# Kernel optimization log

Hardware: AMD Instinct MI355X
Metric: run time of the kernel (lower is better)

Reference implementation:

```python
import jax, jax.numpy as jnp
import numpy as np

LATENT_CH = 64  # feature_ch // 8


def conv1x1(x, w):
    # Conv2dLayer with kernel_size=1, bias=False, activation='linear':
    # weight_gain = 1/sqrt(in_channels * 1)
    gain = 1.0 / np.sqrt(w.shape[1])
    return jnp.einsum('bchw,oc->bohw', x, w * gain)


def casual_attention(q, k, v):
    # q,k,v: [B, C, N] / [B, C, M]; score = q^T k, softmax over keys, out = score @ v^T
    score = jnp.einsum('bcn,bcm->bnm', q, k)
    score = jax.nn.softmax(score, axis=-1)
    return jnp.einsum('bnm,bcm->bnc', score, v)  # [B, N, C]


def reference(feature_map, concepts, w_theta, w_phi, w_g, w_o, gamma_sa, gamma_moca):
    B, C, H, W = feature_map.shape
    L = LATENT_CH
    HW = H * W

    # ---- SelfAttention ----
    th = conv1x1(feature_map, w_theta).reshape(B, L, HW)
    ph = conv1x1(feature_map, w_phi).reshape(B, L, HW)
    g = conv1x1(feature_map, w_g).reshape(B, L, HW)
    # torch does .view(-1, L, H, W) on a [B, HW, L] tensor -> raw memory reinterpret
    lat = casual_attention(th, ph, g).reshape(B, L, H, W)
    sa_out = gamma_sa * conv1x1(lat, w_o) + feature_map

    # ---- MomentumConceptAttention (theta and o shared with SA, trainable_conv=False) ----
    enc = conv1x1(sa_out, w_theta).reshape(B, L, HW)
    phi_c = concepts.T[None]                      # [1, L, P]  (torch.no_grad on concepts)
    phi_c = jnp.broadcast_to(phi_c, (B, L, concepts.shape[0]))
    lat2 = casual_attention(enc, phi_c, phi_c).reshape(B, L, H, W)
    out = gamma_moca * conv1x1(lat2, w_o) + sa_out
    return out


def setup_inputs() -> dict:
    key = jax.random.key(0)
    ks = jax.random.split(key, 8)
    B, C, H, W = 8, 512, 64, 64
    L, P = LATENT_CH, 256
    return {
        'feature_map': jax.random.normal(ks[0], (B, C, H, W), jnp.float32),
        'concepts': jax.random.normal(ks[1], (P, L), jnp.float32),
        'w_theta': jax.random.normal(ks[2], (L, C), jnp.float32),
        'w_phi': jax.random.normal(ks[3], (L, C), jnp.float32),
        'w_g': jax.random.normal(ks[4], (L, C), jnp.float32),
        'w_o': jax.random.normal(ks[5], (C, L), jnp.float32),
        'gamma_sa': jnp.float32(0.1),
        'gamma_moca': jnp.float32(0.1),
    }
```

## Files before the change

### kernel.cpp

```cpp
#include <hip/hip_runtime.h>
#include <math.h>

#define HW   4096
#define CINP 512
#define LCH  64

typedef short bf8 __attribute__((ext_vector_type(8)));
typedef float f4  __attribute__((ext_vector_type(4)));

__device__ __forceinline__ unsigned short f2bf(float x) {
    union { float f; unsigned int u; } v; v.f = x;
    return (unsigned short)((v.u + 0x7fffu + ((v.u >> 16) & 1u)) >> 16);
}
__device__ __forceinline__ bf8 ldbf8(const unsigned short* p) {
    uint4 u = *(const uint4*)p;
    return __builtin_bit_cast(bf8, u);
}

__global__ __launch_bounds__(256) void precast(
    const float* __restrict__ wt, const float* __restrict__ wp,
    const float* __restrict__ wg, const float* __restrict__ wo,
    const float* __restrict__ conc,
    unsigned short* __restrict__ WB, unsigned short* __restrict__ WO,
    unsigned short* __restrict__ CK, unsigned short* __restrict__ CV)
{
    const float gain = 0.04419417382415922f;
    int id = blockIdx.x * 256 + threadIdx.x;
    if (id < 98304) {
        int o = id >> 9, k = id & 511;
        const float* w = (o < 64) ? wt : (o < 128) ? wp : wg;
        WB[id] = f2bf(w[(o & 63) * 512 + k] * gain);
    } else if (id < 131072) {
        int j = id - 98304;
        WO[j] = f2bf(wo[j]);
    } else if (id < 147456) {
        int j = id - 131072;
        CK[j] = f2bf(conc[j]);
    } else if (id < 163840) {
        int j = id - 147456;
        int l = j >> 8, m = j & 255;
        CV[j] = f2bf(conc[m * 64 + l]);
    }
}

__global__ __launch_bounds__(256) void cast_transpose(const float* __restrict__ x,
                                                      unsigned short* __restrict__ XT)
{
    __shared__ unsigned short Lb[64][72];
    const int t  = threadIdx.x;
    const int n0 = blockIdx.x * 64, c0 = blockIdx.y * 64, b = blockIdx.z;
    const float* xb = x + ((size_t)b * CINP + c0) * HW + n0;
    const int cc = t >> 4, n4 = (t & 15) * 4;
    #pragma unroll
    for (int i = 0; i < 4; i++) {
        int c = cc + i * 16;
        float4 v = *(const float4*)(xb + (size_t)c * HW + n4);
        Lb[n4 + 0][c] = f2bf(v.x);
        Lb[n4 + 1][c] = f2bf(v.y);
        Lb[n4 + 2][c] = f2bf(v.z);
        Lb[n4 + 3][c] = f2bf(v.w);
    }
    __syncthreads();
    const int n = t & 63, cb0 = t >> 6;
    unsigned short* orow = XT + ((size_t)b * HW + n0 + n) * CINP + c0;
    #pragma unroll
    for (int i = 0; i < 2; i++) {
        int cb = cb0 + i * 4;
        *(uint4*)(orow + cb * 8) = *(const uint4*)&Lb[n][cb * 8];
    }
}

__global__ __launch_bounds__(256) void lat_transpose(const unsigned short* __restrict__ A,
                                                     unsigned short* __restrict__ LT)
{
    __shared__ unsigned short Ls[64][72];
    const int t = threadIdx.x, s0 = blockIdx.x * 64, b = blockIdx.y;
    const unsigned short* ab = A + (size_t)b * LCH * HW;
    #pragma unroll
    for (int it = 0; it < 2; it++) {
        int c = (t >> 3) + it * 32, s8 = (t & 7) * 8;
        union { uint4 u; unsigned short s[8]; } v;
        v.u = *(const uint4*)(ab + (size_t)c * HW + s0 + s8);
        #pragma unroll
        for (int i = 0; i < 8; i++) Ls[s8 + i][c] = v.s[i];
    }
    __syncthreads();
    unsigned short* ob = LT + ((size_t)b * HW + s0) * LCH;
    #pragma unroll
    for (int it = 0; it < 2; it++) {
        int s = (t >> 3) + it * 32, c8 = (t & 7);
        *(uint4*)(ob + (size_t)s * LCH + c8 * 8) = *(const uint4*)&Ls[s][c8 * 8];
    }
}

template <int NRT>
__global__ __launch_bounds__(256) void qkv_gemm(unsigned short* XT,
                                                const unsigned short* __restrict__ WB,
                                                unsigned short* __restrict__ VL)
{
    const int t = threadIdx.x;
    const int wave = t >> 6, lane = t & 63, quad = lane >> 4, lidx = lane & 15;
    const int b = blockIdx.y;
    const int ncol = blockIdx.x * 64 + wave * 16 + lidx;
    unsigned short* xrow = XT + ((size_t)b * HW + ncol) * CINP;

    f4 acc[NRT];
    #pragma unroll
    for (int r = 0; r < NRT; r++) acc[r] = (f4){0.f, 0.f, 0.f, 0.f};

    for (int kk = 0; kk < 16; kk++) {
        const int k0 = kk * 32 + quad * 8;
        bf8 bq = ldbf8(xrow + k0);
        #pragma unroll
        for (int rt = 0; rt < NRT; rt++) {
            bf8 aw = ldbf8(WB + (size_t)(rt * 16 + lidx) * CINP + k0);
            acc[rt] = __builtin_amdgcn_mfma_f32_16x16x32_bf16(aw, bq, acc[rt], 0, 0, 0);
        }
    }

    #pragma unroll
    for (int rt = 0; rt < NRT; rt++) {
        if (rt < 8) {
            union { unsigned short s[4]; uint2 u; } pk;
            #pragma unroll
            for (int r = 0; r < 4; r++) pk.s[r] = f2bf(acc[rt][r]);
            int off = (rt < 4) ? (rt * 16 + quad * 4) : (64 + (rt - 4) * 16 + quad * 4);
            *(uint2*)(xrow + off) = pk.u;
        } else {
            #pragma unroll
            for (int r = 0; r < 4; r++) {
                int l = (rt - 8) * 16 + quad * 4 + r;
                VL[((size_t)b * LCH + l) * HW + ncol] = f2bf(acc[rt][r]);
            }
        }
    }
}

__global__ __launch_bounds__(64) void flash(
    const unsigned short* Qb, size_t qbat,
    const unsigned short* Kb, size_t krow, size_t kbat,
    const unsigned short* Vb, size_t vrow, size_t vbat,
    unsigned short* __restrict__ Aout, int nkeys)
{
    __shared__ __align__(16) unsigned short Ps[2][32][40];

    const int lane = threadIdx.x, quad = lane >> 4, lidx = lane & 15;
    const int b = blockIdx.y, q0 = blockIdx.x * 32;
    const unsigned short* qp = Qb + (size_t)b * qbat;
    const unsigned short* kp = Kb + (size_t)b * kbat;
    const unsigned short* vp = Vb + (size_t)b * vbat;

    bf8 qa[2][2];
    #pragma unroll
    for (int qb = 0; qb < 2; qb++)
        #pragma unroll
        for (int kh = 0; kh < 2; kh++)
            qa[qb][kh] = ldbf8(qp + (size_t)(q0 + qb * 16 + lidx) * CINP + kh * 32 + quad * 8);

    f4 O[2][4];
    float Lp[2][4];
    #pragma unroll
    for (int qb = 0; qb < 2; qb++) {
        #pragma unroll
        for (int lt = 0; lt < 4; lt++) O[qb][lt] = (f4){0.f, 0.f, 0.f, 0.f};
        #pragma unroll
        for (int r = 0; r < 4; r++) Lp[qb][r] = 0.f;
    }

    const int ntiles = nkeys >> 5;
    #pragma unroll 2
    for (int tl = 0; tl < ntiles; tl++) {
        const int m0 = tl * 32;
        const unsigned short* kr0 = kp + (size_t)(m0 + lidx) * krow + quad * 8;
        const unsigned short* kr1 = kp + (size_t)(m0 + 16 + lidx) * krow + quad * 8;
        bf8 kf00 = ldbf8(kr0), kf01 = ldbf8(kr0 + 32);
        bf8 kf10 = ldbf8(kr1), kf11 = ldbf8(kr1 + 32);

        f4 S[2][2];
        #pragma unroll
        for (int qb = 0; qb < 2; qb++) {
            S[qb][0] = (f4){0.f, 0.f, 0.f, 0.f};
            S[qb][1] = (f4){0.f, 0.f, 0.f, 0.f};
            S[qb][0] = __builtin_amdgcn_mfma_f32_16x16x32_bf16(qa[qb][0], kf00, S[qb][0], 0, 0, 0);
            S[qb][0] = __builtin_amdgcn_mfma_f32_16x16x32_bf16(qa[qb][1], kf01, S[qb][0], 0, 0, 0);
            S[qb][1] = __builtin_amdgcn_mfma_f32_16x16x32_bf16(qa[qb][0], kf10, S[qb][1], 0, 0, 0);
            S[qb][1] = __builtin_amdgcn_mfma_f32_16x16x32_bf16(qa[qb][1], kf11, S[qb][1], 0, 0, 0);
        }

        const int pb = tl & 1;
        #pragma unroll
        for (int qb = 0; qb < 2; qb++)
            #pragma unroll
            for (int ms = 0; ms < 2; ms++)
                #pragma unroll
                for (int r = 0; r < 4; r++) {
                    float p = __expf(S[qb][ms][r]);
                    Lp[qb][r] += p;
                    Ps[pb][qb * 16 + quad * 4 + r][ms * 16 + lidx] = f2bf(p);
                }

        bf8 pf0 = *(const bf8*)&Ps[pb][lidx][quad * 8];
        bf8 pf1 = *(const bf8*)&Ps[pb][16 + lidx][quad * 8];

        #pragma unroll
        for (int lt = 0; lt < 4; lt++) {
            bf8 vf = ldbf8(vp + (size_t)(lt * 16 + lidx) * vrow + m0 + quad * 8);
            O[0][lt] = __builtin_amdgcn_mfma_f32_16x16x32_bf16(pf0, vf, O[0][lt], 0, 0, 0);
            O[1][lt] = __builtin_amdgcn_mfma_f32_16x16x32_bf16(pf1, vf, O[1][lt], 0, 0, 0);
        }
    }

    #pragma unroll
    for (int qb = 0; qb < 2; qb++) {
        float inv[4];
        #pragma unroll
        for (int r = 0; r < 4; r++) {
            float s = Lp[qb][r];
            s += __shfl_xor(s, 1);
            s += __shfl_xor(s, 2);
            s += __shfl_xor(s, 4);
            s += __shfl_xor(s, 8);
            inv[r] = 1.f / s;
        }
        #pragma unroll
        for (int lt = 0; lt < 4; lt++)
            #pragma unroll
            for (int r = 0; r < 4; r++) {
                size_t n = (size_t)b * HW + q0 + qb * 16 + quad * 4 + r;
                Aout[n * LCH + lt * 16 + lidx] = f2bf(O[qb][lt][r] * inv[r]);
            }
    }
}

__global__ __launch_bounds__(256) void conv_o(const unsigned short* __restrict__ LT,
                                              const unsigned short* __restrict__ WO,
                                              const float* __restrict__ res,
                                              const float* __restrict__ gamma_p,
                                              float* __restrict__ out,
                                              unsigned short* ST)
{
    const int t = threadIdx.x;
    const int wave = t >> 6, lane = t & 63, quad = lane >> 4, lidx = lane & 15;
    const int b = blockIdx.z, o0 = blockIdx.y * 64;
    const int scol = blockIdx.x * 64 + wave * 16 + lidx;
    const unsigned short* arow = LT + ((size_t)b * HW + scol) * LCH;

    f4 acc[4];
    #pragma unroll
    for (int ot = 0; ot < 4; ot++) acc[ot] = (f4){0.f, 0.f, 0.f, 0.f};

    #pragma unroll
    for (int kh = 0; kh < 2; kh++) {
        bf8 bq = ldbf8(arow + kh * 32 + quad * 8);
        #pragma unroll
        for (int ot = 0; ot < 4; ot++) {
            bf8 af = ldbf8(WO + (size_t)(o0 + ot * 16 + lidx) * LCH + kh * 32 + quad * 8);
            acc[ot] = __builtin_amdgcn_mfma_f32_16x16x32_bf16(af, bq, acc[ot], 0, 0, 0);
        }
    }

    const float scale = gamma_p[0] * 0.125f;
    #pragma unroll
    for (int ot = 0; ot < 4; ot++) {
        float v[4];
        #pragma unroll
        for (int r = 0; r < 4; r++) {
            size_t idx = ((size_t)b * CINP + o0 + ot * 16 + quad * 4 + r) * HW + scol;
            v[r] = fmaf(scale, acc[ot][r], res[idx]);
            out[idx] = v[r];
        }
        if (ST) {
            union { unsigned short s[4]; uint2 u; } pk;
            #pragma unroll
            for (int r = 0; r < 4; r++) pk.s[r] = f2bf(v[r]);
            *(uint2*)(ST + ((size_t)b * HW + scol) * CINP + o0 + ot * 16 + quad * 4) = pk.u;
        }
    }
}

extern "C" void kernel_launch(void* const* d_in, const int* in_sizes, int n_in,
                              void* d_out, int out_size, void* d_ws, size_t ws_size,
                              hipStream_t stream)
{
    const float* f    = (const float*)d_in[0];
    const float* conc = (const float*)d_in[1];
    const float* wt   = (const float*)d_in[2];
    const float* wp   = (const float*)d_in[3];
    const float* wg   = (const float*)d_in[4];
    const float* wo   = (const float*)d_in[5];
    const float* gsa  = (const float*)d_in[6];
    const float* gmo  = (const float*)d_in[7];
    float* out = (float*)d_out;

    char* ws = (char*)d_ws;
    unsigned short* XT = (unsigned short*)ws;
    unsigned short* VL = (unsigned short*)(ws + ((size_t)32 << 20));
    unsigned short* LT = VL;
    unsigned short* A1 = (unsigned short*)(ws + ((size_t)36 << 20));
    unsigned short* WB = (unsigned short*)(ws + ((size_t)40 << 20));
    unsigned short* WO = WB + 192 * 512;
    unsigned short* CK = WO + 512 * 64;
    unsigned short* CV = CK + 256 * 64;

    dim3 blk256(256), blk64(64);

    precast<<<640, blk256, 0, stream>>>(wt, wp, wg, wo, conc, WB, WO, CK, CV);
    cast_transpose<<<dim3(64, 8, 8), blk256, 0, stream>>>(f, XT);

    qkv_gemm<12><<<dim3(64, 8), blk256, 0, stream>>>(XT, WB, VL);
    flash<<<dim3(128, 8), blk64, 0, stream>>>(
        XT, (size_t)HW * CINP,
        XT + 64, CINP, (size_t)HW * CINP,
        VL, HW, (size_t)LCH * HW,
        A1, HW);
    lat_transpose<<<dim3(64, 8), blk256, 0, stream>>>(A1, LT);
    conv_o<<<dim3(64, 8, 8), blk256, 0, stream>>>(LT, WO, f, gsa, out, XT );

    qkv_gemm<4><<<dim3(64, 8), blk256, 0, stream>>>(XT , WB , nullptr);
    flash<<<dim3(128, 8), blk64, 0, stream>>>(
        XT, (size_t)HW * CINP,
        CK, LCH, 0,
        CV, 256, 0,
        A1 , 256);
    lat_transpose<<<dim3(64, 8), blk256, 0, stream>>>(A1, LT);
    conv_o<<<dim3(64, 8, 8), blk256, 0, stream>>>(LT, WO, out, gmo, out, nullptr);
}
```

Measured before the change: 416.8 us.

## Split flash attention keys across four waves with LDS reduction

The flash kernel now runs 256 threads per block, and each of four waves processes a quarter of the key tiles for the same 32 queries. Partial output accumulators and row sums are written to shared memory and summed by wave 0 before normalization. This raises the number of active waves to better fill the GPU and hide memory latency. In exchange it adds LDS traffic, two block barriers and extra registers, and it only works when the key count divides into 128-key chunks.

```diff
diff --git a/kernel.cpp b/kernel.cpp
--- a/kernel.cpp
+++ b/kernel.cpp
@@ -136,16 +136,21 @@
     }
 }
 
-__global__ __launch_bounds__(64) void flash(
+__global__ __launch_bounds__(256) void flash(
     const unsigned short* Qb, size_t qbat,
     const unsigned short* Kb, size_t krow, size_t kbat,
     const unsigned short* Vb, size_t vrow, size_t vbat,
     unsigned short* __restrict__ Aout, int nkeys)
 {
-    __shared__ __align__(16) unsigned short Ps[2][32][40];
-
-    const int lane = threadIdx.x, quad = lane >> 4, lidx = lane & 15;
+    __shared__ __align__(16) char smem[31488];
+
+    const int t = threadIdx.x;
+    const int wave = t >> 6, lane = t & 63, quad = lane >> 4, lidx = lane & 15;
     const int b = blockIdx.y, q0 = blockIdx.x * 32;
+
+    unsigned short (*Ps)[32][40] = (unsigned short (*)[32][40])(smem + wave * 5120);
+    float (*Red)[64][41] = (float (*)[64][41])smem;
+
     const unsigned short* qp = Qb + (size_t)b * qbat;
     const unsigned short* kp = Kb + (size_t)b * kbat;
     const unsigned short* vp = Vb + (size_t)b * vbat;
@@ -167,10 +172,11 @@
         for (int r = 0; r < 4; r++) Lp[qb][r] = 0.f;
     }
 
-    const int ntiles = nkeys >> 5;
+    const int tpw = nkeys >> 7;
+    const int tbase = wave * tpw;
     #pragma unroll 2
-    for (int tl = 0; tl < ntiles; tl++) {
-        const int m0 = tl * 32;
+    for (int tt = 0; tt < tpw; tt++) {
+        const int m0 = (tbase + tt) * 32;
         const unsigned short* kr0 = kp + (size_t)(m0 + lidx) * krow + quad * 8;
         const unsigned short* kr1 = kp + (size_t)(m0 + 16 + lidx) * krow + quad * 8;
         bf8 kf00 = ldbf8(kr0), kf01 = ldbf8(kr0 + 32);
@@ -187,7 +193,7 @@
             S[qb][1] = __builtin_amdgcn_mfma_f32_16x16x32_bf16(qa[qb][1], kf11, S[qb][1], 0, 0, 0);
         }
 
-        const int pb = tl & 1;
+        const int pb = tt & 1;
         #pragma unroll
         for (int qb = 0; qb < 2; qb++)
             #pragma unroll
@@ -210,25 +216,59 @@
         }
     }
 
-    #pragma unroll
-    for (int qb = 0; qb < 2; qb++) {
-        float inv[4];
-        #pragma unroll
-        for (int r = 0; r < 4; r++) {
-            float s = Lp[qb][r];
-            s += __shfl_xor(s, 1);
-            s += __shfl_xor(s, 2);
-            s += __shfl_xor(s, 4);
-            s += __shfl_xor(s, 8);
-            inv[r] = 1.f / s;
-        }
-        #pragma unroll
-        for (int lt = 0; lt < 4; lt++)
+    __syncthreads();
+    if (wave) {
+        float* rp = Red[wave - 1][lane];
+        int j = 0;
+        #pragma unroll
+        for (int qb = 0; qb < 2; qb++)
+            #pragma unroll
+            for (int lt = 0; lt < 4; lt++)
+                #pragma unroll
+                for (int r = 0; r < 4; r++) rp[j++] = O[qb][lt][r];
+        #pragma unroll
+        for (int qb = 0; qb < 2; qb++)
+            #pragma unroll
+            for (int r = 0; r < 4; r++) rp[32 + qb * 4 + r] = Lp[qb][r];
+    }
+    __syncthreads();
+    if (wave == 0) {
+        #pragma unroll
+        for (int w = 0; w < 3; w++) {
+            const float* rp = Red[w][lane];
+            int j = 0;
+            #pragma unroll
+            for (int qb = 0; qb < 2; qb++)
+                #pragma unroll
+                for (int lt = 0; lt < 4; lt++)
+                    #pragma unroll
+                    for (int r = 0; r < 4; r++) O[qb][lt][r] += rp[j++];
+            #pragma unroll
+            for (int qb = 0; qb < 2; qb++)
+                #pragma unroll
+                for (int r = 0; r < 4; r++) Lp[qb][r] += rp[32 + qb * 4 + r];
+        }
+
+        #pragma unroll
+        for (int qb = 0; qb < 2; qb++) {
+            float inv[4];
             #pragma unroll
             for (int r = 0; r < 4; r++) {
-                size_t n = (size_t)b * HW + q0 + qb * 16 + quad * 4 + r;
-                Aout[n * LCH + lt * 16 + lidx] = f2bf(O[qb][lt][r] * inv[r]);
+                float s = Lp[qb][r];
+                s += __shfl_xor(s, 1);
+                s += __shfl_xor(s, 2);
+                s += __shfl_xor(s, 4);
+                s += __shfl_xor(s, 8);
+                inv[r] = 1.f / s;
             }
+            #pragma unroll
+            for (int lt = 0; lt < 4; lt++)
+                #pragma unroll
+                for (int r = 0; r < 4; r++) {
+                    size_t n = (size_t)b * HW + q0 + qb * 16 + quad * 4 + r;
+                    Aout[n * LCH + lt * 16 + lidx] = f2bf(O[qb][lt][r] * inv[r]);
+                }
+        }
     }
 }
 
@@ -302,13 +342,13 @@
     unsigned short* CK = WO + 512 * 64;
     unsigned short* CV = CK + 256 * 64;
 
-    dim3 blk256(256), blk64(64);
+    dim3 blk256(256);
 
     precast<<<640, blk256, 0, stream>>>(wt, wp, wg, wo, conc, WB, WO, CK, CV);
     cast_transpose<<<dim3(64, 8, 8), blk256, 0, stream>>>(f, XT);
 
     qkv_gemm<12><<<dim3(64, 8), blk256, 0, stream>>>(XT, WB, VL);
-    flash<<<dim3(128, 8), blk64, 0, stream>>>(
+    flash<<<dim3(128, 8), blk256, 0, stream>>>(
         XT, (size_t)HW * CINP,
         XT + 64, CINP, (size_t)HW * CINP,
         VL, HW, (size_t)LCH * HW,
@@ -317,7 +357,7 @@
     conv_o<<<dim3(64, 8, 8), blk256, 0, stream>>>(LT, WO, f, gsa, out, XT );
 
     qkv_gemm<4><<<dim3(64, 8), blk256, 0, stream>>>(XT , WB , nullptr);
-    flash<<<dim3(128, 8), blk64, 0, stream>>>(
+    flash<<<dim3(128, 8), blk256, 0, stream>>>(
         XT, (size_t)HW * CINP,
         CK, LCH, 0,
         CV, 256, 0,
```

Result: slower. 425.9 us (+2.2%).

## Share K/V tiles across four waves via double-buffered LDS in flash kernel

Applied to the files above, without the earlier changes.

The flash attention kernel now runs four waves per block, each owning 32 query rows, and the block cooperatively loads each 32-key K and V tile into double-buffered shared memory with a prefetch of the next tile. This replaces per-wave global loads of K/V, cutting global/L2 traffic by up to four times. It also swaps the S MFMA operand order so P is written transposed with packed bf16 conversion (v_cvt_pk_bf16_f32), and the row-sum reduction shrinks to two shuffles. It adds a __syncthreads per tile, more LDS per block, and a grid of only 256 blocks, which may limit occupancy on a large GPU.

```diff
diff --git a/kernel.cpp b/kernel.cpp
--- a/kernel.cpp
+++ b/kernel.cpp
@@ -15,6 +15,11 @@
 __device__ __forceinline__ bf8 ldbf8(const unsigned short* p) {
     uint4 u = *(const uint4*)p;
     return __builtin_bit_cast(bf8, u);
+}
+__device__ __forceinline__ unsigned int cvtpk(float a, float b) {
+    unsigned int r;
+    asm volatile("v_cvt_pk_bf16_f32 %0, %1, %2" : "=v"(r) : "v"(a), "v"(b));
+    return r;
 }
 
 __global__ __launch_bounds__(256) void precast(
@@ -136,20 +141,27 @@
     }
 }
 
-__global__ __launch_bounds__(64) void flash(
+__global__ __launch_bounds__(256) void flash(
     const unsigned short* Qb, size_t qbat,
     const unsigned short* Kb, size_t krow, size_t kbat,
     const unsigned short* Vb, size_t vrow, size_t vbat,
     unsigned short* __restrict__ Aout, int nkeys)
 {
-    __shared__ __align__(16) unsigned short Ps[2][32][40];
-
-    const int lane = threadIdx.x, quad = lane >> 4, lidx = lane & 15;
-    const int b = blockIdx.y, q0 = blockIdx.x * 32;
+    __shared__ __align__(16) unsigned short Ks[2][32][72];
+    __shared__ __align__(16) unsigned short Vs[2][64][40];
+    __shared__ __align__(16) unsigned short Ps[4][32][40];
+
+    const int t = threadIdx.x;
+    const int wave = t >> 6, lane = t & 63, quad = lane >> 4, lidx = lane & 15;
+    const int b = blockIdx.y, q0 = blockIdx.x * 128 + wave * 32;
+
     const unsigned short* qp = Qb + (size_t)b * qbat;
     const unsigned short* kp = Kb + (size_t)b * kbat;
     const unsigned short* vp = Vb + (size_t)b * vbat;
 
+    const int krt = t >> 3, kch = (t & 7) * 8;
+    const int vrt = t >> 2, vch = (t & 3) * 8;
+
     bf8 qa[2][2];
     #pragma unroll
     for (int qb = 0; qb < 2; qb++)
@@ -158,78 +170,99 @@
             qa[qb][kh] = ldbf8(qp + (size_t)(q0 + qb * 16 + lidx) * CINP + kh * 32 + quad * 8);
 
     f4 O[2][4];
-    float Lp[2][4];
-    #pragma unroll
-    for (int qb = 0; qb < 2; qb++) {
+    float Lp[2] = {0.f, 0.f};
+    #pragma unroll
+    for (int qb = 0; qb < 2; qb++)
         #pragma unroll
         for (int lt = 0; lt < 4; lt++) O[qb][lt] = (f4){0.f, 0.f, 0.f, 0.f};
-        #pragma unroll
-        for (int r = 0; r < 4; r++) Lp[qb][r] = 0.f;
-    }
-
-    const int ntiles = nkeys >> 5;
-    #pragma unroll 2
-    for (int tl = 0; tl < ntiles; tl++) {
-        const int m0 = tl * 32;
-        const unsigned short* kr0 = kp + (size_t)(m0 + lidx) * krow + quad * 8;
-        const unsigned short* kr1 = kp + (size_t)(m0 + 16 + lidx) * krow + quad * 8;
-        bf8 kf00 = ldbf8(kr0), kf01 = ldbf8(kr0 + 32);
-        bf8 kf10 = ldbf8(kr1), kf11 = ldbf8(kr1 + 32);
+
+    const int nt = nkeys >> 5;
+
+    {
+        uint4 k0v = *(const uint4*)(kp + (size_t)krt * krow + kch);
+        uint4 v0v = *(const uint4*)(vp + (size_t)vrt * vrow + vch);
+        *(uint4*)&Ks[0][krt][kch] = k0v;
+        *(uint4*)&Vs[0][vrt][vch] = v0v;
+    }
+    __syncthreads();
+
+    for (int tl = 0; tl < nt; tl++) {
+        const int cur = tl & 1;
+        const bool pf = (tl + 1 < nt);
+        uint4 kpre, vpre;
+        if (pf) {
+            const int m1 = (tl + 1) * 32;
+            kpre = *(const uint4*)(kp + (size_t)(m1 + krt) * krow + kch);
+            vpre = *(const uint4*)(vp + (size_t)vrt * vrow + m1 + vch);
+        }
+
+        bf8 kf[2][2];
+        #pragma unroll
+        for (int ms = 0; ms < 2; ms++)
+            #pragma unroll
+            for (int kh = 0; kh < 2; kh++)
+                kf[ms][kh] = *(const bf8*)&Ks[cur][ms * 16 + lidx][kh * 32 + quad * 8];
 
         f4 S[2][2];
         #pragma unroll
-        for (int qb = 0; qb < 2; qb++) {
-            S[qb][0] = (f4){0.f, 0.f, 0.f, 0.f};
-            S[qb][1] = (f4){0.f, 0.f, 0.f, 0.f};
-            S[qb][0] = __builtin_amdgcn_mfma_f32_16x16x32_bf16(qa[qb][0], kf00, S[qb][0], 0, 0, 0);
-            S[qb][0] = __builtin_amdgcn_mfma_f32_16x16x32_bf16(qa[qb][1], kf01, S[qb][0], 0, 0, 0);
-            S[qb][1] = __builtin_amdgcn_mfma_f32_16x16x32_bf16(qa[qb][0], kf10, S[qb][1], 0, 0, 0);
-            S[qb][1] = __builtin_amdgcn_mfma_f32_16x16x32_bf16(qa[qb][1], kf11, S[qb][1], 0, 0, 0);
-        }
-
-        const int pb = tl & 1;
-        #pragma unroll
         for (int qb = 0; qb < 2; qb++)
             #pragma unroll
-            for (int ms = 0; ms < 2; ms++)
-                #pragma unroll
-                for (int r = 0; r < 4; r++) {
-                    float p = __expf(S[qb][ms][r]);
-                    Lp[qb][r] += p;
-                    Ps[pb][qb * 16 + quad * 4 + r][ms * 16 + lidx] = f2bf(p);
-                }
-
-        bf8 pf0 = *(const bf8*)&Ps[pb][lidx][quad * 8];
-        bf8 pf1 = *(const bf8*)&Ps[pb][16 + lidx][quad * 8];
-
+            for (int ms = 0; ms < 2; ms++) {
+                f4 s = (f4){0.f, 0.f, 0.f, 0.f};
+                s = __builtin_amdgcn_mfma_f32_16x16x32_bf16(kf[ms][0], qa[qb][0], s, 0, 0, 0);
+                s = __builtin_amdgcn_mfma_f32_16x16x32_bf16(kf[ms][1], qa[qb][1], s, 0, 0, 0);
+                S[qb][ms] = s;
+            }
+
+        #pragma unroll
+        for (int qb = 0; qb < 2; qb++)
+            #pragma unroll
+            for (int ms = 0; ms < 2; ms++) {
+                float p0 = __expf(S[qb][ms][0]);
+                float p1 = __expf(S[qb][ms][1]);
+                float p2 = __expf(S[qb][ms][2]);
+                float p3 = __expf(S[qb][ms][3]);
+                Lp[qb] += (p0 + p1) + (p2 + p3);
+                uint2 pk;
+                pk.x = cvtpk(p0, p1);
+                pk.y = cvtpk(p2, p3);
+                *(uint2*)&Ps[wave][qb * 16 + lidx][ms * 16 + quad * 4] = pk;
+            }
+
+        bf8 pf0 = *(const bf8*)&Ps[wave][lidx][quad * 8];
+        bf8 pf1 = *(const bf8*)&Ps[wave][16 + lidx][quad * 8];
         #pragma unroll
         for (int lt = 0; lt < 4; lt++) {
-            bf8 vf = ldbf8(vp + (size_t)(lt * 16 + lidx) * vrow + m0 + quad * 8);
+            bf8 vf = *(const bf8*)&Vs[cur][lt * 16 + lidx][quad * 8];
             O[0][lt] = __builtin_amdgcn_mfma_f32_16x16x32_bf16(pf0, vf, O[0][lt], 0, 0, 0);
             O[1][lt] = __builtin_amdgcn_mfma_f32_16x16x32_bf16(pf1, vf, O[1][lt], 0, 0, 0);
         }
-    }
-
+
+        if (pf) {
+            *(uint4*)&Ks[cur ^ 1][krt][kch] = kpre;
+            *(uint4*)&Vs[cur ^ 1][vrt][vch] = vpre;
+        }
+        __syncthreads();
+    }
+
+    float inv[2];
     #pragma unroll
     for (int qb = 0; qb < 2; qb++) {
-        float inv[4];
+        float s = Lp[qb];
+        s += __shfl_xor(s, 16);
+        s += __shfl_xor(s, 32);
+        inv[qb] = 1.f / s;
+    }
+    #pragma unroll
+    for (int qb = 0; qb < 2; qb++)
         #pragma unroll
         for (int r = 0; r < 4; r++) {
-            float s = Lp[qb][r];
-            s += __shfl_xor(s, 1);
-            s += __shfl_xor(s, 2);
-            s += __shfl_xor(s, 4);
-            s += __shfl_xor(s, 8);
-            inv[r] = 1.f / s;
-        }
-        #pragma unroll
-        for (int lt = 0; lt < 4; lt++)
-            #pragma unroll
-            for (int r = 0; r < 4; r++) {
-                size_t n = (size_t)b * HW + q0 + qb * 16 + quad * 4 + r;
-                Aout[n * LCH + lt * 16 + lidx] = f2bf(O[qb][lt][r] * inv[r]);
-            }
-    }
+            float iv = __shfl(inv[qb], quad * 4 + r);
+            size_t n = (size_t)b * HW + q0 + qb * 16 + quad * 4 + r;
+            #pragma unroll
+            for (int lt = 0; lt < 4; lt++)
+                Aout[n * LCH + lt * 16 + lidx] = f2bf(O[qb][lt][r] * iv);
+        }
 }
 
 __global__ __launch_bounds__(256) void conv_o(const unsigned short* __restrict__ LT,
@@ -302,13 +335,13 @@
     unsigned short* CK = WO + 512 * 64;
     unsigned short* CV = CK + 256 * 64;
 
-    dim3 blk256(256), blk64(64);
+    dim3 blk256(256);
 
     precast<<<640, blk256, 0, stream>>>(wt, wp, wg, wo, conc, WB, WO, CK, CV);
     cast_transpose<<<dim3(64, 8, 8), blk256, 0, stream>>>(f, XT);
 
     qkv_gemm<12><<<dim3(64, 8), blk256, 0, stream>>>(XT, WB, VL);
-    flash<<<dim3(128, 8), blk64, 0, stream>>>(
+    flash<<<dim3(32, 8), blk256, 0, stream>>>(
         XT, (size_t)HW * CINP,
         XT + 64, CINP, (size_t)HW * CINP,
         VL, HW, (size_t)LCH * HW,
@@ -317,7 +350,7 @@
     conv_o<<<dim3(64, 8, 8), blk256, 0, stream>>>(LT, WO, f, gsa, out, XT );
 
     qkv_gemm<4><<<dim3(64, 8), blk256, 0, stream>>>(XT , WB , nullptr);
-    flash<<<dim3(128, 8), blk64, 0, stream>>>(
+    flash<<<dim3(32, 8), blk256, 0, stream>>>(
         XT, (size_t)HW * CINP,
         CK, LCH, 0,
         CV, 256, 0,
```

Result: faster. 397.2 us (-4.7%).
